# Optimization experiments

Measured on AMD Instinct MI355X. Metric: run time of the kernel, lower is better.

Reference implementation:

```python
import jax, jax.numpy as jnp
import numpy as np

FS = 512.0
T = 2048
CYC_PHA, CYC_AMP = 3, 6
NBINS = 18
PHA_BANDS = [(2.0 + 2.0 * k, 4.0 + 2.0 * k) for k in range(10)]
AMP_BANDS = [(30.0 + 12.0 * k, 42.0 + 12.0 * k) for k in range(10)]


def _design_filter(fs, low, high, cycle):
    # windowed-sinc bandpass, taps = cycle * fs / low (tensorpac cycle rule), forced odd
    n = int(cycle * fs / low)
    if n % 2 == 0:
        n += 1
    t = np.arange(n) - (n - 1) / 2.0
    lp = lambda fc: 2.0 * fc / fs * np.sinc(2.0 * fc / fs * t)
    h = (lp(high) - lp(low)) * np.hamming(n)
    fc = 0.5 * (low + high)
    h = h / np.abs(np.sum(h * np.exp(-2j * np.pi * fc / fs * t)))  # unit gain at band center
    return h.astype(np.float32)


def _build_kernels():
    filts = [_design_filter(FS, l, h, CYC_PHA) for l, h in PHA_BANDS] + \
            [_design_filter(FS, l, h, CYC_AMP) for l, h in AMP_BANDS]
    L = max(f.shape[0] for f in filts)
    padded = []
    for f in filts:
        p = L - f.shape[0]
        pl = p // 2
        padded.append(np.pad(f, (pl, p - pl)))
    return np.stack(padded)  # (F, L), L odd


def _conv_same(sig, kernels):
    # sig: (N, Tp), kernels: (F, L) -> (N, F, Tp); cross-correlation, 'same' padding (L odd)
    L = kernels.shape[1]
    pad = (L - 1) // 2
    return jax.lax.conv_general_dilated(
        sig[:, None, :], kernels[:, None, :], window_strides=(1,),
        padding=((pad, L - 1 - pad),), dimension_numbers=("NCH", "OIH", "NCH"))


def _analytic(x):
    # FFT-based Hilbert analytic signal along last axis
    n = x.shape[-1]
    h = np.zeros(n, np.float32)
    h[0] = 1.0
    if n % 2 == 0:
        h[n // 2] = 1.0
        h[1:n // 2] = 2.0
    else:
        h[1:(n + 1) // 2] = 2.0
    return jnp.fft.ifft(jnp.fft.fft(x, axis=-1) * h, axis=-1)


def _modulation_index(pha, amp):
    # Tort MI: pha (B,C,P,S,T), amp (B,C,A,S,T) -> (B,C,P,A)
    idx = jnp.clip(jnp.floor((pha + jnp.pi) / (2.0 * jnp.pi) * NBINS), 0, NBINS - 1).astype(jnp.int32)
    sums, cnts = [], []
    for b in range(NBINS):  # fixed small bin count
        m = (idx == b).astype(amp.dtype)                       # (B,C,P,S,T)
        sums.append(jnp.einsum('bcpst,bcast->bcpas', m, amp))  # (B,C,P,A,S)
        cnts.append(m.sum(-1))                                 # (B,C,P,S)
    amp_sum = jnp.stack(sums, -1)                              # (B,C,P,A,S,N)
    cnt = jnp.stack(cnts, -1)[:, :, :, None, :, :]             # (B,C,P,1,S,N)
    amp_mean = amp_sum / jnp.maximum(cnt, 1.0)
    p = amp_mean / jnp.maximum(amp_mean.sum(-1, keepdims=True), 1e-12)
    log_n = jnp.log(jnp.asarray(NBINS, amp.dtype))
    mi = (log_n + (p * jnp.log(jnp.maximum(p, 1e-12))).sum(-1)) / log_n
    return mi.mean(-1)  # average over segments


def setup_inputs() -> dict:
    key = jax.random.key(0)
    x = jax.random.normal(key, (4, 8, 4, T), dtype=jnp.float32)
    kernels = jnp.asarray(_build_kernels())
    return {"x": x, "kernels": kernels}


def reference(x, kernels):
    B, C, S, Tlen = x.shape
    npha = len(PHA_BANDS)
    pad = kernels.shape[1] - 1  # max_padlen (edge_mode)
    sig = x.reshape(B * C * S, Tlen)
    sig = jnp.pad(sig, ((0, 0), (pad, pad)), mode='reflect')
    # filtfilt_mode: average forward conv and time-reversed conv
    fwd = _conv_same(sig, kernels)
    bwd = _conv_same(sig[:, ::-1], kernels)[:, :, ::-1]
    filt = 0.5 * (fwd + bwd)
    filt = filt[:, :, pad:-pad]  # strip edge padding -> (N, F, T)
    ana = _analytic(filt)
    pha = jnp.arctan2(ana.imag[:, :npha], ana.real[:, :npha])
    amp = jnp.sqrt(ana.real[:, npha:] ** 2 + ana.imag[:, npha:] ** 2)
    pha = pha.reshape(B, C, npha, S, Tlen)
    amp = amp.reshape(B, C, len(AMP_BANDS), S, Tlen)
    return _modulation_index(pha, amp)
```

## Files before the change

kernel.cpp:

```cpp
#include <hip/hip_runtime.h>
#include <math.h>

#define TT 2048
#define LK 769
#define NF 20
#define NS 128
#define NB 18

typedef __attribute__((ext_vector_type(8))) short short8;
typedef __attribute__((ext_vector_type(4))) float f32x4;

__global__ __launch_bounds__(256) void prep_kernel(const float* __restrict__ ker,
                                                   float2* __restrict__ tw,
                                                   float* __restrict__ hsym,
                                                   int* __restrict__ rng) {
  __shared__ int red[4][2];
  const int blk = blockIdx.x;
  const int tid = threadIdx.x;
  if (blk < 8) {
    int i = blk * 256 + tid;
    if (i == 0) { tw[0] = make_float2(1.f, 0.f); }
    else {
      int half = 1 << (31 - __clz(i));
      int j = i - half;
      float ang = -3.14159265358979323846f * (float)j / (float)half;
      float s, c;
      sincosf(ang, &s, &c);
      tw[i] = make_float2(c, s);
    }
    return;
  }
  const int o = blk - 8;
  const float* kr = ker + o * LK;
  int k0 = 784, k1 = 0;
  for (int k = tid; k < 784; k += 256) {
    float v = 0.f;
    if (k < LK) v = 0.5f * (kr[k] + kr[LK - 1 - k]);
    hsym[o * 784 + k] = v;
    if (v != 0.f) { k0 = min(k0, k); k1 = max(k1, k + 1); }
  }
#pragma unroll
  for (int off = 32; off > 0; off >>= 1) {
    k0 = min(k0, __shfl_down(k0, off));
    k1 = max(k1, __shfl_down(k1, off));
  }
  if ((tid & 63) == 0) { red[tid >> 6][0] = k0; red[tid >> 6][1] = k1; }
  __syncthreads();
  if (tid == 0) {
    k0 = min(min(red[0][0], red[1][0]), min(red[2][0], red[3][0]));
    k1 = max(max(red[0][1], red[1][1]), max(red[2][1], red[3][1]));
    rng[2 * o] = k0 & ~7;
    rng[2 * o + 1] = (k1 + 7) & ~7;
  }
}

__global__ __launch_bounds__(256) void convhil_kernel(const float* __restrict__ x,
                                                      const float* __restrict__ hsym,
                                                      const int* __restrict__ rng,
                                                      const float2* __restrict__ tw,
                                                      float* __restrict__ filt) {
  __shared__ __align__(16) float smem[4400];
  float* w   = smem;
  float* hs1 = smem + 2832;
  float* hs2 = smem + 3616;
  float2* z  = (float2*)smem;
  const int tid = threadIdx.x;
  const int ord = blockIdx.x;
  const int p = ord / NS;
  const int n = ord % NS;
  const int o1 = p;
  const int o2 = 10 + (9 - p);
  const float* xr = x + n * TT;
  for (int j = tid; j < 2832; j += 256) {
    float v = 0.f;
    if (j < 2816) {
      int m = j - 384;
      if (m < 0) m = -m;
      if (m > 2047) m = 4094 - m;
      v = xr[m];
    }
    w[j] = v;
  }
  const float* h1g = hsym + o1 * 784;
  const float* h2g = hsym + o2 * 784;
  for (int k = tid; k < 784; k += 256) {
    hs1[k] = h1g[k];
    hs2[k] = h2g[k];
  }
  const int A0 = rng[2 * o1], A1 = rng[2 * o1 + 1];
  const int B0 = rng[2 * o2], B1 = rng[2 * o2 + 1];
  const int U0 = min(A0, B0);
  const int U1 = max(A1, B1);
  __syncthreads();

  const int bA = 4 * tid;
  const int bB = 1024 + 4 * tid;
  float acc1A[4], acc1B[4], acc2A[4], acc2B[4];
#pragma unroll
  for (int r = 0; r < 4; ++r) { acc1A[r] = 0.f; acc1B[r] = 0.f; acc2A[r] = 0.f; acc2B[r] = 0.f; }
  if (U0 < U1) {
    float4 a0 = *(const float4*)&w[bA + U0];
    float4 a1 = *(const float4*)&w[bA + U0 + 4];
    float4 a2 = *(const float4*)&w[bA + U0 + 8];
    float4 b0 = *(const float4*)&w[bB + U0];
    float4 b1 = *(const float4*)&w[bB + U0 + 4];
    float4 b2 = *(const float4*)&w[bB + U0 + 8];
    float4 h1a = *(const float4*)&hs1[U0];
    float4 h1b = *(const float4*)&hs1[U0 + 4];
    float4 h2a = *(const float4*)&hs2[U0];
    float4 h2b = *(const float4*)&hs2[U0 + 4];
    for (int k = U0; k < U1; k += 8) {
      float4 a3 = *(const float4*)&w[bA + k + 12];
      float4 a4 = *(const float4*)&w[bA + k + 16];
      float4 b3 = *(const float4*)&w[bB + k + 12];
      float4 b4 = *(const float4*)&w[bB + k + 16];
      float4 h1an = *(const float4*)&hs1[k + 8];
      float4 h1bn = *(const float4*)&hs1[k + 12];
      float4 h2an = *(const float4*)&hs2[k + 8];
      float4 h2bn = *(const float4*)&hs2[k + 12];
      float wa[11] = {a0.x, a0.y, a0.z, a0.w, a1.x, a1.y, a1.z, a1.w,
                      a2.x, a2.y, a2.z};
      float wb[11] = {b0.x, b0.y, b0.z, b0.w, b1.x, b1.y, b1.z, b1.w,
                      b2.x, b2.y, b2.z};
      float h1[8] = {h1a.x, h1a.y, h1a.z, h1a.w, h1b.x, h1b.y, h1b.z, h1b.w};
      float h2[8] = {h2a.x, h2a.y, h2a.z, h2a.w, h2b.x, h2b.y, h2b.z, h2b.w};
      if (k >= A0 && k < A1) {
#pragma unroll
        for (int r = 0; r < 4; ++r) {
#pragma unroll
          for (int j = 0; j < 8; ++j) {
            acc1A[r] = fmaf(h1[j], wa[r + j], acc1A[r]);
            acc1B[r] = fmaf(h1[j], wb[r + j], acc1B[r]);
          }
        }
      }
      if (k >= B0 && k < B1) {
#pragma unroll
        for (int r = 0; r < 4; ++r) {
#pragma unroll
          for (int j = 0; j < 8; ++j) {
            acc2A[r] = fmaf(h2[j], wa[r + j], acc2A[r]);
            acc2B[r] = fmaf(h2[j], wb[r + j], acc2B[r]);
          }
        }
      }
      a0 = a2; a1 = a3; a2 = a4;
      b0 = b2; b1 = b3; b2 = b4;
      h1a = h1an; h1b = h1bn;
      h2a = h2an; h2b = h2bn;
    }
  }
  __syncthreads();
#pragma unroll
  for (int r = 0; r < 4; ++r) {
    z[bA + r] = make_float2(acc1A[r], acc2A[r]);
    z[bB + r] = make_float2(acc1B[r], acc2B[r]);
  }
  __syncthreads();
  for (int bf = tid; bf < 1024; bf += 256) {
    const float2 t = tw[1024 + bf];
    const float2 u = z[bf];
    const float2 v = z[bf + 1024];
    z[bf] = make_float2(u.x + v.x, u.y + v.y);
    const float dr = u.x - v.x, di = u.y - v.y;
    z[bf + 1024] = make_float2(fmaf(t.x, dr, -(t.y * di)),
                               fmaf(t.x, di, t.y * dr));
  }
  __syncthreads();
  for (int Q = 256; Q >= 1; Q >>= 2) {
    for (int bf = tid; bf < 512; bf += 256) {
      const int j = bf & (Q - 1);
      const int base = ((bf & ~(Q - 1)) << 2) + j;
      const float2 x0 = z[base], x1 = z[base + Q];
      const float2 x2 = z[base + 2 * Q], x3 = z[base + 3 * Q];
      const float2 w1 = tw[2 * Q + j];
      const float2 w2 = tw[Q + j];
      const float w3r = w1.x * w2.x - w1.y * w2.y;
      const float w3i = w1.x * w2.y + w1.y * w2.x;
      const float t0r = x0.x + x2.x, t0i = x0.y + x2.y;
      const float t1r = x0.x - x2.x, t1i = x0.y - x2.y;
      const float t2r = x1.x + x3.x, t2i = x1.y + x3.y;
      const float t3r = x1.x - x3.x, t3i = x1.y - x3.y;
      z[base] = make_float2(t0r + t2r, t0i + t2i);
      const float a1r = t1r + t3i, a1i = t1i - t3r;
      z[base + Q] = make_float2(a1r * w1.x - a1i * w1.y,
                                a1r * w1.y + a1i * w1.x);
      const float a2r = t0r - t2r, a2i = t0i - t2i;
      z[base + 2 * Q] = make_float2(a2r * w2.x - a2i * w2.y,
                                    a2r * w2.y + a2i * w2.x);
      const float a3r = t1r - t3i, a3i = t1i + t3r;
      z[base + 3 * Q] = make_float2(a3r * w3r - a3i * w3i,
                                    a3r * w3i + a3i * w3r);
    }
    __syncthreads();
  }
  for (int pp = tid; pp < TT; pp += 256) {
    if (pp != 0 && pp != 2) {
      if (pp & 2) { z[pp] = make_float2(0.f, 0.f); }
      else        { float2 v = z[pp]; z[pp] = make_float2(2.f * v.x, 2.f * v.y); }
    }
  }
  __syncthreads();
  for (int Q = 1; Q <= 256; Q <<= 2) {
    for (int bf = tid; bf < 512; bf += 256) {
      const int j = bf & (Q - 1);
      const int base = ((bf & ~(Q - 1)) << 2) + j;
      const float2 y0 = z[base], y1 = z[base + Q];
      const float2 y2 = z[base + 2 * Q], y3 = z[base + 3 * Q];
      const float2 w1 = tw[2 * Q + j];
      const float2 w2 = tw[Q + j];
      const float w3r = w1.x * w2.x - w1.y * w2.y;
      const float w3i = w1.x * w2.y + w1.y * w2.x;
      const float u1r = y1.x * w1.x + y1.y * w1.y;
      const float u1i = y1.y * w1.x - y1.x * w1.y;
      const float u2r = y2.x * w2.x + y2.y * w2.y;
      const float u2i = y2.y * w2.x - y2.x * w2.y;
      const float u3r = y3.x * w3r + y3.y * w3i;
      const float u3i = y3.y * w3r - y3.x * w3i;
      const float t0r = y0.x + u2r, t0i = y0.y + u2i;
      const float t1r = y0.x - u2r, t1i = y0.y - u2i;
      const float t2r = u1r + u3r, t2i = u1i + u3i;
      const float t3r = u1r - u3r, t3i = u1i - u3i;
      z[base]         = make_float2(t0r + t2r, t0i + t2i);
      z[base + Q]     = make_float2(t1r - t3i, t1i + t3r);
      z[base + 2 * Q] = make_float2(t0r - t2r, t0i - t2i);
      z[base + 3 * Q] = make_float2(t1r + t3i, t1i - t3r);
    }
    __syncthreads();
  }
  for (int bf = tid; bf < 1024; bf += 256) {
    const float2 t = tw[1024 + bf];
    const float2 u = z[bf];
    const float2 v = z[bf + 1024];
    const float vr = v.x * t.x + v.y * t.y;
    const float vi = v.y * t.x - v.x * t.y;
    z[bf] = make_float2(u.x + vr, u.y + vi);
    z[bf + 1024] = make_float2(u.x - vr, u.y - vi);
  }
  __syncthreads();
  float* out1 = filt + ((size_t)n * NF + o1) * TT;
  float* out2 = filt + ((size_t)n * NF + o2) * TT;
  const float invN = 1.0f / 2048.0f;
  float phA[4], phB[4], amA[4], amB[4];
#pragma unroll
  for (int r = 0; r < 4; ++r) {
    float2 wvA = z[bA + r];
    float h1 = wvA.y * invN - acc2A[r];
    float h2 = acc1A[r] - wvA.x * invN;
    phA[r] = atan2f(h1, acc1A[r]);
    amA[r] = sqrtf(fmaf(acc2A[r], acc2A[r], h2 * h2));
    float2 wvB = z[bB + r];
    float g1 = wvB.y * invN - acc2B[r];
    float g2 = acc1B[r] - wvB.x * invN;
    phB[r] = atan2f(g1, acc1B[r]);
    amB[r] = sqrtf(fmaf(acc2B[r], acc2B[r], g2 * g2));
  }
  *(float4*)&out1[bA] = make_float4(phA[0], phA[1], phA[2], phA[3]);
  *(float4*)&out1[bB] = make_float4(phB[0], phB[1], phB[2], phB[3]);
  *(float4*)&out2[bA] = make_float4(amA[0], amA[1], amA[2], amA[3]);
  *(float4*)&out2[bB] = make_float4(amB[0], amB[1], amB[2], amB[3]);
}

__global__ __launch_bounds__(256) void mi_kernel(const float* __restrict__ filt,
                                                 float* __restrict__ mi) {
  __shared__ __align__(16) unsigned int idx32[512];
  __shared__ float Cp[4][12][19];
  const int tid = threadIdx.x;
  const int wave = tid >> 6;
  const int lane = tid & 63;
  const int blk = blockIdx.x;
  const int bc = blk / 40, jp = blk % 40;
  const float* ph = filt + ((size_t)(bc * 4 + jp / 10) * NF + (jp % 10)) * TT;
  for (int g = tid; g < 512; g += 256) {
    float4 v = *(const float4*)&ph[4 * g];
    float vv[4] = {v.x, v.y, v.z, v.w};
    unsigned int packed = 0;
#pragma unroll
    for (int j = 0; j < 4; ++j) {
      int b = (int)floorf((vv[j] + 3.14159274f) / 6.2831855f * 18.0f);
      b = b < 0 ? 0 : (b > 17 ? 17 : b);
      packed |= ((unsigned int)b) << (8 * j);
    }
    idx32[g] = packed;
  }
  __syncthreads();
  const int n16 = lane & 15;
  const int quad = lane >> 4;
  const int aband = n16 < 10 ? n16 : 9;
  const int ja = (jp & 3) + 4 * aband;
  const float* aptr = filt + ((size_t)(bc * 4 + ja / 10) * NF + 10 + (ja % 10)) * TT
                      + quad * 8;
  const bool isAmp = (n16 < 10);
  const bool isOne = (n16 == 10);
  f32x4 acc0 = {0.f, 0.f, 0.f, 0.f};
  f32x4 acc1 = {0.f, 0.f, 0.f, 0.f};
  const int s0 = wave * 16, s1 = s0 + 16;
  float4 p0 = *(const float4*)(aptr + s0 * 32);
  float4 p1 = *(const float4*)(aptr + s0 * 32 + 4);
  for (int s = s0; s < s1; ++s) {
    float4 c0 = p0, c1 = p1;
    if (s < s1 - 1) {
      p0 = *(const float4*)(aptr + (s + 1) * 32);
      p1 = *(const float4*)(aptr + (s + 1) * 32 + 4);
    }
    float a[8] = {c0.x, c0.y, c0.z, c0.w, c1.x, c1.y, c1.z, c1.w};
    short8 ah, am_, al;
#pragma unroll
    for (int j = 0; j < 8; ++j) {
      float v = isAmp ? a[j] : (isOne ? 1.0f : 0.0f);
      unsigned int u = __float_as_uint(v);
      float h = __uint_as_float(u & 0xFFFF0000u);
      float r1 = v - h;
      unsigned int u2 = __float_as_uint(r1);
      float md = __uint_as_float(u2 & 0xFFFF0000u);
      float r2 = r1 - md;
      unsigned int u3 = __float_as_uint(r2);
      ah[j] = (short)(u >> 16);
      am_[j] = (short)(u2 >> 16);
      al[j] = (short)(u3 >> 16);
    }
    const int dw = s * 8 + quad * 2;
    unsigned int d0 = idx32[dw], d1 = idx32[dw + 1];
    short8 b0, b1;
#pragma unroll
    for (int j = 0; j < 8; ++j) {
      unsigned int byte = ((j < 4 ? d0 : d1) >> ((j & 3) * 8)) & 0xFFu;
      b0[j] = (byte == (unsigned int)n16) ? (short)0x3F80 : (short)0;
      b1[j] = (byte == (unsigned int)(n16 + 16)) ? (short)0x3F80 : (short)0;
    }
    acc0 = __builtin_amdgcn_mfma_f32_16x16x32_bf16(ah, b0, acc0, 0, 0, 0);
    acc0 = __builtin_amdgcn_mfma_f32_16x16x32_bf16(am_, b0, acc0, 0, 0, 0);
    acc0 = __builtin_amdgcn_mfma_f32_16x16x32_bf16(al, b0, acc0, 0, 0, 0);
    acc1 = __builtin_amdgcn_mfma_f32_16x16x32_bf16(ah, b1, acc1, 0, 0, 0);
    acc1 = __builtin_amdgcn_mfma_f32_16x16x32_bf16(am_, b1, acc1, 0, 0, 0);
    acc1 = __builtin_amdgcn_mfma_f32_16x16x32_bf16(al, b1, acc1, 0, 0, 0);
  }
#pragma unroll
  for (int r = 0; r < 4; ++r) {
    int row = quad * 4 + r;
    if (row < 11) {
      Cp[wave][row][n16] = acc0[r];
      if (n16 < 2) Cp[wave][row][16 + n16] = acc1[r];
    }
  }
  __syncthreads();
  if (tid < 10) {
    float tot = 0.f, mb_[18];
#pragma unroll
    for (int b = 0; b < 18; ++b) {
      float s = Cp[0][tid][b] + Cp[1][tid][b] + Cp[2][tid][b] + Cp[3][tid][b];
      float c = Cp[0][10][b] + Cp[1][10][b] + Cp[2][10][b] + Cp[3][10][b];
      float mb = s / fmaxf(c, 1.0f);
      mb_[b] = mb; tot += mb;
    }
    tot = fmaxf(tot, 1e-12f);
    float s = 0.f;
#pragma unroll
    for (int b = 0; b < 18; ++b) {
      float pb = mb_[b] / tot;
      s += pb * logf(fmaxf(pb, 1e-12f));
    }
    const float LOGN = 2.8903717578961645f;
    mi[(size_t)blk * 10 + tid] = (LOGN + s) / LOGN;
  }
}

__global__ void out_kernel(const float* __restrict__ mi, float* __restrict__ out) {
  int i = blockIdx.x * 256 + threadIdx.x;
  if (i < 3200) {
    int a = i % 10, p = (i / 10) % 10, bc = i / 100;
    float s = 0.f;
    for (int sp = 0; sp < 4; ++sp)
      s += mi[((size_t)(bc * 40 + p * 4 + sp)) * 10 + a];
    out[i] = 0.25f * s;
  }
}

extern "C" void kernel_launch(void* const* d_in, const int* in_sizes, int n_in,
                              void* d_out, int out_size, void* d_ws, size_t ws_size,
                              hipStream_t stream) {
  (void)in_sizes; (void)n_in; (void)out_size; (void)ws_size;
  const float* x = (const float*)d_in[0];
  const float* ker = (const float*)d_in[1];
  float* out = (float*)d_out;
  float* filt = (float*)d_ws;
  float* mi = filt + (size_t)NS * NF * TT;
  float2* tw = (float2*)(mi + 12800);
  float* hsym = (float*)(tw + TT);
  int* rng = (int*)(hsym + NF * 784);

  prep_kernel<<<28, 256, 0, stream>>>(ker, tw, hsym, rng);
  convhil_kernel<<<NS * 10, 256, 0, stream>>>(x, hsym, rng, tw, filt);
  mi_kernel<<<32 * 40, 256, 0, stream>>>(filt, mi);
  out_kernel<<<(3200 + 255) / 256, 256, 0, stream>>>(mi, out);
}
```

Baseline: 139.4 us.

## Emit phase bins and bf16-split amplitudes from conv kernel instead of floats

The conv/Hilbert kernel now computes the phase bin index and the three-way bf16 split of amplitude directly, writing packed byte bins and three bf16 planes instead of fp32 phase/amplitude. The MI kernel loads these MFMA-ready operands directly, dropping its shared-memory binning pass and per-element split arithmetic. Intermediate traffic shifts from 8 bytes per sample-pair to about 7 bytes, and the MI loop drops its manual prefetch in favour of unroll 4. The split work is not duplicated across the phase bands that reuse each amplitude row, but it adds workspace layout changes.

New measurement: 142.1 us. About the same (+2.0%).

```diff
diff --git a/kernel.cpp b/kernel.cpp
--- a/kernel.cpp
+++ b/kernel.cpp
@@ -54,11 +54,28 @@
   }
 }
 
+__device__ __forceinline__ void split3(float v, unsigned short& h,
+                                       unsigned short& m, unsigned short& l) {
+  unsigned int u = __float_as_uint(v);
+  float hf = __uint_as_float(u & 0xFFFF0000u);
+  float r1 = v - hf;
+  unsigned int u2 = __float_as_uint(r1);
+  float mf = __uint_as_float(u2 & 0xFFFF0000u);
+  float r2 = r1 - mf;
+  unsigned int u3 = __float_as_uint(r2);
+  h = (unsigned short)(u >> 16);
+  m = (unsigned short)(u2 >> 16);
+  l = (unsigned short)(u3 >> 16);
+}
+
 __global__ __launch_bounds__(256) void convhil_kernel(const float* __restrict__ x,
                                                       const float* __restrict__ hsym,
                                                       const int* __restrict__ rng,
                                                       const float2* __restrict__ tw,
-                                                      float* __restrict__ filt) {
+                                                      unsigned short* __restrict__ asH,
+                                                      unsigned short* __restrict__ asM,
+                                                      unsigned short* __restrict__ asL,
+                                                      unsigned char* __restrict__ idx8) {
   __shared__ __align__(16) float smem[4400];
   float* w   = smem;
   float* hs1 = smem + 2832;
@@ -238,89 +255,78 @@
     z[bf + 1024] = make_float2(u.x - vr, u.y - vi);
   }
   __syncthreads();
-  float* out1 = filt + ((size_t)n * NF + o1) * TT;
-  float* out2 = filt + ((size_t)n * NF + o2) * TT;
   const float invN = 1.0f / 2048.0f;
-  float phA[4], phB[4], amA[4], amB[4];
-#pragma unroll
-  for (int r = 0; r < 4; ++r) {
-    float2 wvA = z[bA + r];
-    float h1 = wvA.y * invN - acc2A[r];
-    float h2 = acc1A[r] - wvA.x * invN;
-    phA[r] = atan2f(h1, acc1A[r]);
-    amA[r] = sqrtf(fmaf(acc2A[r], acc2A[r], h2 * h2));
-    float2 wvB = z[bB + r];
-    float g1 = wvB.y * invN - acc2B[r];
-    float g2 = acc1B[r] - wvB.x * invN;
-    phB[r] = atan2f(g1, acc1B[r]);
-    amB[r] = sqrtf(fmaf(acc2B[r], acc2B[r], g2 * g2));
-  }
-  *(float4*)&out1[bA] = make_float4(phA[0], phA[1], phA[2], phA[3]);
-  *(float4*)&out1[bB] = make_float4(phB[0], phB[1], phB[2], phB[3]);
-  *(float4*)&out2[bA] = make_float4(amA[0], amA[1], amA[2], amA[3]);
-  *(float4*)&out2[bB] = make_float4(amB[0], amB[1], amB[2], amB[3]);
-}
-
-__global__ __launch_bounds__(256) void mi_kernel(const float* __restrict__ filt,
+  const size_t ibase = ((size_t)n * 10 + p) * TT;
+  const size_t abase = ((size_t)n * 10 + (9 - p)) * TT;
+#pragma unroll
+  for (int g = 0; g < 2; ++g) {
+    const int base = g ? bB : bA;
+    const float* a1 = g ? acc1B : acc1A;
+    const float* a2 = g ? acc2B : acc2A;
+    unsigned int binpack = 0;
+    unsigned short hh[4], mm[4], ll[4];
+#pragma unroll
+    for (int r = 0; r < 4; ++r) {
+      float2 wv = z[base + r];
+      float h1 = wv.y * invN - a2[r];
+      float h2 = a1[r] - wv.x * invN;
+      float ph = atan2f(h1, a1[r]);
+      float am = sqrtf(fmaf(a2[r], a2[r], h2 * h2));
+      int b = (int)floorf((ph + 3.14159274f) / 6.2831855f * 18.0f);
+      b = b < 0 ? 0 : (b > 17 ? 17 : b);
+      binpack |= ((unsigned int)b) << (8 * r);
+      split3(am, hh[r], mm[r], ll[r]);
+    }
+    *(unsigned int*)(idx8 + ibase + base) = binpack;
+    uint2 ph2, pm2, pl2;
+    ph2.x = (unsigned int)hh[0] | ((unsigned int)hh[1] << 16);
+    ph2.y = (unsigned int)hh[2] | ((unsigned int)hh[3] << 16);
+    pm2.x = (unsigned int)mm[0] | ((unsigned int)mm[1] << 16);
+    pm2.y = (unsigned int)mm[2] | ((unsigned int)mm[3] << 16);
+    pl2.x = (unsigned int)ll[0] | ((unsigned int)ll[1] << 16);
+    pl2.y = (unsigned int)ll[2] | ((unsigned int)ll[3] << 16);
+    *(uint2*)(asH + abase + base) = ph2;
+    *(uint2*)(asM + abase + base) = pm2;
+    *(uint2*)(asL + abase + base) = pl2;
+  }
+}
+
+__global__ __launch_bounds__(256) void mi_kernel(const unsigned short* __restrict__ asH,
+                                                 const unsigned short* __restrict__ asM,
+                                                 const unsigned short* __restrict__ asL,
+                                                 const unsigned char* __restrict__ idx8,
                                                  float* __restrict__ mi) {
-  __shared__ __align__(16) unsigned int idx32[512];
   __shared__ float Cp[4][12][19];
   const int tid = threadIdx.x;
   const int wave = tid >> 6;
   const int lane = tid & 63;
   const int blk = blockIdx.x;
   const int bc = blk / 40, jp = blk % 40;
-  const float* ph = filt + ((size_t)(bc * 4 + jp / 10) * NF + (jp % 10)) * TT;
-  for (int g = tid; g < 512; g += 256) {
-    float4 v = *(const float4*)&ph[4 * g];
-    float vv[4] = {v.x, v.y, v.z, v.w};
-    unsigned int packed = 0;
-#pragma unroll
-    for (int j = 0; j < 4; ++j) {
-      int b = (int)floorf((vv[j] + 3.14159274f) / 6.2831855f * 18.0f);
-      b = b < 0 ? 0 : (b > 17 ? 17 : b);
-      packed |= ((unsigned int)b) << (8 * j);
-    }
-    idx32[g] = packed;
-  }
-  __syncthreads();
   const int n16 = lane & 15;
   const int quad = lane >> 4;
   const int aband = n16 < 10 ? n16 : 9;
   const int ja = (jp & 3) + 4 * aband;
-  const float* aptr = filt + ((size_t)(bc * 4 + ja / 10) * NF + 10 + (ja % 10)) * TT
-                      + quad * 8;
+  const size_t arow = (size_t)((bc * 4 + ja / 10) * 10 + (ja % 10)) * TT + quad * 8;
+  const size_t prow = (size_t)((bc * 4 + jp / 10) * 10 + (jp % 10)) * TT;
+  const unsigned char* ib = idx8 + prow + quad * 8;
   const bool isAmp = (n16 < 10);
   const bool isOne = (n16 == 10);
   f32x4 acc0 = {0.f, 0.f, 0.f, 0.f};
   f32x4 acc1 = {0.f, 0.f, 0.f, 0.f};
   const int s0 = wave * 16, s1 = s0 + 16;
-  float4 p0 = *(const float4*)(aptr + s0 * 32);
-  float4 p1 = *(const float4*)(aptr + s0 * 32 + 4);
+#pragma unroll 4
   for (int s = s0; s < s1; ++s) {
-    float4 c0 = p0, c1 = p1;
-    if (s < s1 - 1) {
-      p0 = *(const float4*)(aptr + (s + 1) * 32);
-      p1 = *(const float4*)(aptr + (s + 1) * 32 + 4);
-    }
-    float a[8] = {c0.x, c0.y, c0.z, c0.w, c1.x, c1.y, c1.z, c1.w};
-    short8 ah, am_, al;
-#pragma unroll
-    for (int j = 0; j < 8; ++j) {
-      float v = isAmp ? a[j] : (isOne ? 1.0f : 0.0f);
-      unsigned int u = __float_as_uint(v);
-      float h = __uint_as_float(u & 0xFFFF0000u);
-      float r1 = v - h;
-      unsigned int u2 = __float_as_uint(r1);
-      float md = __uint_as_float(u2 & 0xFFFF0000u);
-      float r2 = r1 - md;
-      unsigned int u3 = __float_as_uint(r2);
-      ah[j] = (short)(u >> 16);
-      am_[j] = (short)(u2 >> 16);
-      al[j] = (short)(u3 >> 16);
-    }
-    const int dw = s * 8 + quad * 2;
-    unsigned int d0 = idx32[dw], d1 = idx32[dw + 1];
+    const size_t o = arow + (size_t)s * 32;
+    short8 ah = *(const short8*)(asH + o);
+    short8 am_ = *(const short8*)(asM + o);
+    short8 al = *(const short8*)(asL + o);
+    if (!isAmp) {
+      const short ov = isOne ? (short)0x3F80 : (short)0;
+#pragma unroll
+      for (int j = 0; j < 8; ++j) { ah[j] = ov; am_[j] = 0; al[j] = 0; }
+    }
+    const uint2 d = *(const uint2*)(ib + s * 32);
+    const unsigned int d0 = d.x, d1 = d.y;
     short8 b0, b1;
 #pragma unroll
     for (int j = 0; j < 8; ++j) {
@@ -383,14 +389,18 @@
   const float* x = (const float*)d_in[0];
   const float* ker = (const float*)d_in[1];
   float* out = (float*)d_out;
-  float* filt = (float*)d_ws;
-  float* mi = filt + (size_t)NS * NF * TT;
+
+  float* mi = (float*)d_ws;
   float2* tw = (float2*)(mi + 12800);
   float* hsym = (float*)(tw + TT);
   int* rng = (int*)(hsym + NF * 784);
+  unsigned short* asH = (unsigned short*)(rng + 40);
+  unsigned short* asM = asH + (size_t)NS * 10 * TT;
+  unsigned short* asL = asM + (size_t)NS * 10 * TT;
+  unsigned char* idx8 = (unsigned char*)(asL + (size_t)NS * 10 * TT);
 
   prep_kernel<<<28, 256, 0, stream>>>(ker, tw, hsym, rng);
-  convhil_kernel<<<NS * 10, 256, 0, stream>>>(x, hsym, rng, tw, filt);
-  mi_kernel<<<32 * 40, 256, 0, stream>>>(filt, mi);
+  convhil_kernel<<<NS * 10, 256, 0, stream>>>(x, hsym, rng, tw, asH, asM, asL, idx8);
+  mi_kernel<<<32 * 40, 256, 0, stream>>>(asH, asM, asL, idx8, mi);
   out_kernel<<<(3200 + 255) / 256, 256, 0, stream>>>(mi, out);
 }
```
